# Optimization experiments

Hardware: AMD Instinct MI355X
Metric: run time of the kernel (lower is better)

## Reference

```python
import jax, jax.numpy as jnp
import numpy as np

N_HEADS = 16
KEY_DIM = 64
VAL_DIM = 64
KV_CH = 512


def setup_inputs() -> dict:
    key = jax.random.key(0)
    k1, k2, k3, k4, k5, k6 = jax.random.split(key, 6)
    B, H, W = 32, 64, 64
    kv = jax.random.normal(k1, (B, H, W, KV_CH), dtype=jnp.float32)
    # 1x1 conv kernels are just [C_in, C_out] matrices
    scale = 1.0 / np.sqrt(KV_CH)
    W_k = jax.random.normal(k2, (KV_CH, N_HEADS * KEY_DIM), dtype=jnp.float32) * scale
    b_k = jnp.zeros((N_HEADS * KEY_DIM,), dtype=jnp.float32)
    W_v = jax.random.normal(k3, (KV_CH, N_HEADS * VAL_DIM), dtype=jnp.float32) * scale
    b_v = jnp.zeros((N_HEADS * VAL_DIM,), dtype=jnp.float32)
    query = jax.random.normal(k4, (1, 1, N_HEADS, KEY_DIM), dtype=jnp.float32) * 0.05
    return {"key_value": kv, "W_k": W_k, "b_k": b_k, "W_v": W_v, "b_v": b_v, "query": query}


def reference(key_value, W_k, b_k, W_v, b_v, query):
    B, H, W, _ = key_value.shape
    HW = H * W
    x = key_value.reshape(B, HW, KV_CH)  # 1x1 conv == per-pixel matmul
    key = (jnp.einsum('bsc,cd->bsd', x, W_k) + b_k).reshape(B, HW, N_HEADS, KEY_DIM)
    value = jnp.tanh(jnp.einsum('bsc,cd->bsd', x, W_v) + b_v).reshape(B, HW, N_HEADS, VAL_DIM)
    # query broadcast dot over key dim -> [B, HW, N]
    dot = jnp.einsum('bsnk,nk->bsn', key, query[0, 0])
    attn = jax.nn.softmax(dot, axis=1)  # softmax over spatial axis
    # inference mode: dropout is identity
    out = jnp.einsum('bsn,bsnv->bnv', attn, value)  # [B, N, V]
    return out
```

## Files before the change

kernel.cpp:

```cpp
#include <hip/hip_runtime.h>
#include <cstdint>

using short8 = __attribute__((ext_vector_type(8))) short;
using f32x4  = __attribute__((ext_vector_type(4))) float;

__device__ __forceinline__ unsigned short bf16rne(float f) {
  unsigned int u = __float_as_uint(f);
  unsigned int r = u + 0x7fffu + ((u >> 16) & 1u);
  return (unsigned short)(r >> 16);
}

__device__ __forceinline__ void gl2lds16(const void* g, void* s) {
  auto gp = reinterpret_cast<const __attribute__((address_space(1))) unsigned int*>(
      reinterpret_cast<uintptr_t>(g));
  auto sp = reinterpret_cast<__attribute__((address_space(3))) unsigned int*>(
      (uint32_t)reinterpret_cast<uintptr_t>(s));
  __builtin_amdgcn_global_load_lds(gp, sp, 16, 0, 0);
}

__device__ __forceinline__ float fast_tanh(float x) {
  float e = __expf(2.0f * x);
  return 1.0f - 2.0f / (e + 1.0f);
}

__global__ void prep_kernel(const float* __restrict__ Wk, const float* __restrict__ q,
                            const float* __restrict__ Wv,
                            unsigned short* __restrict__ wqb,
                            unsigned short* __restrict__ wvt) {
  int idx = blockIdx.x * 256 + threadIdx.x;
  if (idx < 8192) {
    int n = idx >> 9, c = idx & 511;
    const float* wrow = Wk + (long)c * 1024 + n * 64;
    const float* qrow = q + n * 64;
    float s = 0.f;
    #pragma unroll 8
    for (int k = 0; k < 64; ++k) s += wrow[k] * qrow[k];
    wqb[n * 512 + c] = bf16rne(s);
  } else {
    int j = idx - 8192;
    if (j < 524288) {
      int col = j >> 9, c = j & 511;
      wvt[col * 512 + c] = bf16rne(Wv[(long)c * 1024 + col]);
    }
  }
}

__global__ void convert_kernel(const float4* __restrict__ x, ushort4* __restrict__ xb, int n4) {
  int stride = gridDim.x * blockDim.x;
  for (int i = blockIdx.x * blockDim.x + threadIdx.x; i < n4; i += stride) {
    float4 f = x[i];
    ushort4 o;
    o.x = bf16rne(f.x); o.y = bf16rne(f.y); o.z = bf16rne(f.z); o.w = bf16rne(f.w);
    xb[i] = o;
  }
}

__global__ __launch_bounds__(256) void dot_kernel(
    const unsigned short* __restrict__ xb, const unsigned short* __restrict__ wqb,
    float* __restrict__ dotbuf) {
  __shared__ __align__(16) unsigned short As[128 * 64];
  __shared__ __align__(16) unsigned short Ws[16 * 512];
  int tid = threadIdx.x;
  int l = tid & 63, w = tid >> 6;
  int lr = l >> 3, lc = l & 7;
  long row0 = (long)blockIdx.x * 128;

  for (int j = 0; j < 4; ++j) {
    int n = w * 4 + j;
    gl2lds16(wqb + n * 512 + ((l ^ (n & 7)) * 8), &Ws[n * 512]);
  }

  f32x4 acc[2];
  for (int mi = 0; mi < 2; ++mi) acc[mi] = f32x4{0.f, 0.f, 0.f, 0.f};

  for (int kb = 0; kb < 8; ++kb) {
    __syncthreads();
    for (int j = 0; j < 4; ++j) {
      int jj = w * 4 + j;
      int m = jj * 8 + lr;
      gl2lds16(xb + (row0 + m) * 512 + kb * 64 + ((lc ^ lr) * 8), &As[jj * 512]);
    }
    __syncthreads();
    #pragma unroll
    for (int k32 = 0; k32 < 2; ++k32) {
      int n = l & 15, qd = l >> 4;
      int cl = kb * 8 + k32 * 4 + qd;
      short8 bf = *(const short8*)&Ws[n * 512 + ((cl ^ (n & 7)) * 8)];
      int ch = k32 * 4 + qd;
      #pragma unroll
      for (int mi = 0; mi < 2; ++mi) {
        int m = w * 32 + mi * 16 + (l & 15);
        short8 af = *(const short8*)&As[m * 64 + ((ch ^ (l & 7)) * 8)];
        acc[mi] = __builtin_amdgcn_mfma_f32_16x16x32_bf16(af, bf, acc[mi], 0, 0, 0);
      }
    }
  }
  int n = l & 15, qd = l >> 4;
  for (int mi = 0; mi < 2; ++mi) {
    long rg = row0 + w * 32 + mi * 16 + qd * 4;
    long b = rg >> 12;
    long s = rg & 4095;
    *(f32x4*)&dotbuf[((b * 16 + n) << 12) + s] = acc[mi];
  }
}

__global__ __launch_bounds__(256) void softmax_kernel(float* __restrict__ dotbuf) {
  long bn = blockIdx.x;
  float4* p = (float4*)(dotbuf + bn * 4096);
  int tid = threadIdx.x;
  int l = tid & 63, w = tid >> 6;
  float4 v[4];
  float mx = -1e30f;
  #pragma unroll
  for (int i = 0; i < 4; ++i) {
    v[i] = p[tid + i * 256];
    mx = fmaxf(mx, fmaxf(fmaxf(v[i].x, v[i].y), fmaxf(v[i].z, v[i].w)));
  }
  for (int o = 32; o; o >>= 1) mx = fmaxf(mx, __shfl_xor(mx, o, 64));
  __shared__ float redm[4];
  __shared__ float reds[4];
  if (l == 0) redm[w] = mx;
  __syncthreads();
  mx = fmaxf(fmaxf(redm[0], redm[1]), fmaxf(redm[2], redm[3]));
  float s = 0.f;
  #pragma unroll
  for (int i = 0; i < 4; ++i) {
    v[i].x = __expf(v[i].x - mx); v[i].y = __expf(v[i].y - mx);
    v[i].z = __expf(v[i].z - mx); v[i].w = __expf(v[i].w - mx);
    s += v[i].x + v[i].y + v[i].z + v[i].w;
  }
  for (int o = 32; o; o >>= 1) s += __shfl_xor(s, o, 64);
  if (l == 0) reds[w] = s;
  __syncthreads();
  s = reds[0] + reds[1] + reds[2] + reds[3];
  float inv = 1.0f / s;
  #pragma unroll
  for (int i = 0; i < 4; ++i) {
    v[i].x *= inv; v[i].y *= inv; v[i].z *= inv; v[i].w *= inv;
    p[tid + i * 256] = v[i];
  }
}

__global__ __launch_bounds__(256) void out_gemm_kernel(
    const unsigned short* __restrict__ xb, const unsigned short* __restrict__ wvt,
    const float* __restrict__ wn, const float* __restrict__ bv,
    float* __restrict__ out) {
  __shared__ __align__(16) unsigned short As[128 * 64];
  __shared__ __align__(16) unsigned short Bs[128 * 64];
  __shared__ float wlds[256];
  int tid = threadIdx.x;
  int l = tid & 63, w = tid >> 6;
  int wr = w >> 1, wc = w & 1;
  int lr = l >> 3, lc = l & 7;
  int ct = blockIdx.x, rt = blockIdx.y, b = blockIdx.z;
  long row0 = ((long)b << 12) + rt * 128;
  long col0 = (long)ct * 128;
  const unsigned short* Ag = xb + row0 * 512;
  const unsigned short* Bg = wvt + col0 * 512;

  f32x4 acc[4][4];
  #pragma unroll
  for (int mi = 0; mi < 4; ++mi)
    #pragma unroll
    for (int ni = 0; ni < 4; ++ni) acc[mi][ni] = f32x4{0.f, 0.f, 0.f, 0.f};

  for (int kb = 0; kb < 8; ++kb) {
    __syncthreads();
    for (int j = 0; j < 4; ++j) {
      int jj = w * 4 + j;
      int r = jj * 8 + lr;
      int goff = r * 512 + kb * 64 + (lc ^ lr) * 8;
      gl2lds16(Ag + goff, &As[jj * 512]);
      gl2lds16(Bg + goff, &Bs[jj * 512]);
    }
    __syncthreads();
    #pragma unroll
    for (int k32 = 0; k32 < 2; ++k32) {
      int ch = k32 * 4 + (l >> 4);
      short8 af[4], bfr[4];
      #pragma unroll
      for (int mi = 0; mi < 4; ++mi) {
        int m = wr * 64 + mi * 16 + (l & 15);
        af[mi] = *(const short8*)&As[m * 64 + ((ch ^ (l & 7)) * 8)];
      }
      #pragma unroll
      for (int ni = 0; ni < 4; ++ni) {
        int n = wc * 64 + ni * 16 + (l & 15);
        bfr[ni] = *(const short8*)&Bs[n * 64 + ((ch ^ (l & 7)) * 8)];
      }
      #pragma unroll
      for (int mi = 0; mi < 4; ++mi)
        #pragma unroll
        for (int ni = 0; ni < 4; ++ni)
          acc[mi][ni] = __builtin_amdgcn_mfma_f32_16x16x32_bf16(af[mi], bfr[ni], acc[mi][ni], 0, 0, 0);
    }
  }

  int head0 = ct * 2;
  __syncthreads();
  {
    int hh = tid >> 7, r = tid & 127;
    wlds[tid] = wn[(((long)b * 16 + head0 + hh) << 12) + rt * 128 + r];
  }
  __syncthreads();
  int ngl = head0 + wc;
  int v0 = l & 15, qd = l >> 4;
  float bias[4];
  #pragma unroll
  for (int ni = 0; ni < 4; ++ni) bias[ni] = bv[ngl * 64 + ni * 16 + v0];
  float res[4] = {0.f, 0.f, 0.f, 0.f};
  #pragma unroll
  for (int mi = 0; mi < 4; ++mi) {
    int rb = wr * 64 + mi * 16 + qd * 4;
    float w0 = wlds[wc * 128 + rb + 0];
    float w1 = wlds[wc * 128 + rb + 1];
    float w2 = wlds[wc * 128 + rb + 2];
    float w3 = wlds[wc * 128 + rb + 3];
    #pragma unroll
    for (int ni = 0; ni < 4; ++ni) {
      f32x4 c = acc[mi][ni];
      res[ni] += w0 * fast_tanh(c[0] + bias[ni]) + w1 * fast_tanh(c[1] + bias[ni])
               + w2 * fast_tanh(c[2] + bias[ni]) + w3 * fast_tanh(c[3] + bias[ni]);
    }
  }
  #pragma unroll
  for (int ni = 0; ni < 4; ++ni) {
    float v = res[ni];
    v += __shfl_xor(v, 16, 64);
    v += __shfl_xor(v, 32, 64);
    if (qd == 0) atomicAdd(&out[b * 1024 + ngl * 64 + ni * 16 + v0], v);
  }
}

extern "C" void kernel_launch(void* const* d_in, const int* in_sizes, int n_in,
                              void* d_out, int out_size, void* d_ws, size_t ws_size,
                              hipStream_t stream) {
  const float* kv = (const float*)d_in[0];
  const float* Wk = (const float*)d_in[1];
  const float* Wv = (const float*)d_in[3];
  const float* bv = (const float*)d_in[4];
  const float* q  = (const float*)d_in[5];
  float* out = (float*)d_out;

  char* ws = (char*)d_ws;
  unsigned short* xb  = (unsigned short*)(ws);
  unsigned short* wqb = (unsigned short*)(ws + 134217728);
  unsigned short* wvt = (unsigned short*)(ws + 134217728 + 16384);
  float* dotbuf = (float*)(ws + 134217728 + 16384 + 1048576);

  hipMemsetAsync(d_out, 0, 32768 * sizeof(float), stream);
  prep_kernel<<<2081, 256, 0, stream>>>(Wk, q, Wv, wqb, wvt);
  convert_kernel<<<4096, 256, 0, stream>>>((const float4*)kv, (ushort4*)xb, 16777216);
  dot_kernel<<<1024, 256, 0, stream>>>(xb, wqb, dotbuf);
  softmax_kernel<<<512, 256, 0, stream>>>(dotbuf);
  out_gemm_kernel<<<dim3(8, 32, 32), 256, 0, stream>>>(xb, wvt, dotbuf, bv, out);
}
```

Measured before the change: 656.9 us.

## Fuse fp32-to-bf16 conversion into dot kernel, tile-transpose Wv, swizzle GEMM grid

Drops the separate convert kernel. The dot kernel now reads fp32 activations directly, converts them to bf16 in registers, writes the bf16 copy for the later GEMM, and fills LDS itself, which removes one full read of the large intermediate. The Wv transpose in prep now goes through a padded LDS tile so both its reads and writes are coalesced. The output GEMM grid is flattened and remapped so that blocks sharing the same activation rows run close together, which should improve L2 reuse. The cost is that the dot kernel loses the async global-to-LDS path and gains an extra barrier per K-step.

```diff
diff --git a/kernel.cpp b/kernel.cpp
--- a/kernel.cpp
+++ b/kernel.cpp
@@ -23,12 +23,14 @@
   return 1.0f - 2.0f / (e + 1.0f);
 }
 
-__global__ void prep_kernel(const float* __restrict__ Wk, const float* __restrict__ q,
-                            const float* __restrict__ Wv,
-                            unsigned short* __restrict__ wqb,
-                            unsigned short* __restrict__ wvt) {
-  int idx = blockIdx.x * 256 + threadIdx.x;
-  if (idx < 8192) {
+__global__ __launch_bounds__(256) void prep_kernel(
+    const float* __restrict__ Wk, const float* __restrict__ q,
+    const float* __restrict__ Wv,
+    unsigned short* __restrict__ wqb, unsigned short* __restrict__ wvt) {
+  __shared__ float T[64 * 65];
+  int bid = blockIdx.x;
+  if (bid < 32) {
+    int idx = bid * 256 + threadIdx.x;
     int n = idx >> 9, c = idx & 511;
     const float* wrow = Wk + (long)c * 1024 + n * 64;
     const float* qrow = q + n * 64;
@@ -37,32 +39,31 @@
     for (int k = 0; k < 64; ++k) s += wrow[k] * qrow[k];
     wqb[n * 512 + c] = bf16rne(s);
   } else {
-    int j = idx - 8192;
-    if (j < 524288) {
-      int col = j >> 9, c = j & 511;
-      wvt[col * 512 + c] = bf16rne(Wv[(long)c * 1024 + col]);
-    }
-  }
-}
-
-__global__ void convert_kernel(const float4* __restrict__ x, ushort4* __restrict__ xb, int n4) {
-  int stride = gridDim.x * blockDim.x;
-  for (int i = blockIdx.x * blockDim.x + threadIdx.x; i < n4; i += stride) {
-    float4 f = x[i];
-    ushort4 o;
-    o.x = bf16rne(f.x); o.y = bf16rne(f.y); o.z = bf16rne(f.z); o.w = bf16rne(f.w);
-    xb[i] = o;
+    int t = bid - 32;
+    int tc = t & 7, tl = t >> 3;
+    int c0 = tc * 64, l0 = tl * 64;
+    int j = threadIdx.x & 63, i0 = threadIdx.x >> 6;
+    #pragma unroll
+    for (int ii = 0; ii < 16; ++ii) {
+      int i = i0 * 16 + ii;
+      T[i * 65 + j] = Wv[(long)(c0 + i) * 1024 + l0 + j];
+    }
+    __syncthreads();
+    #pragma unroll
+    for (int ii = 0; ii < 16; ++ii) {
+      int jj = i0 * 16 + ii;
+      wvt[(long)(l0 + jj) * 512 + c0 + j] = bf16rne(T[j * 65 + jj]);
+    }
   }
 }
 
 __global__ __launch_bounds__(256) void dot_kernel(
-    const unsigned short* __restrict__ xb, const unsigned short* __restrict__ wqb,
-    float* __restrict__ dotbuf) {
+    const float* __restrict__ kv, const unsigned short* __restrict__ wqb,
+    unsigned short* __restrict__ xb, float* __restrict__ dotbuf) {
   __shared__ __align__(16) unsigned short As[128 * 64];
   __shared__ __align__(16) unsigned short Ws[16 * 512];
   int tid = threadIdx.x;
   int l = tid & 63, w = tid >> 6;
-  int lr = l >> 3, lc = l & 7;
   long row0 = (long)blockIdx.x * 128;
 
   for (int j = 0; j < 4; ++j) {
@@ -74,11 +75,29 @@
   for (int mi = 0; mi < 2; ++mi) acc[mi] = f32x4{0.f, 0.f, 0.f, 0.f};
 
   for (int kb = 0; kb < 8; ++kb) {
-    __syncthreads();
-    for (int j = 0; j < 4; ++j) {
-      int jj = w * 4 + j;
-      int m = jj * 8 + lr;
-      gl2lds16(xb + (row0 + m) * 512 + kb * 64 + ((lc ^ lr) * 8), &As[jj * 512]);
+    float4 fa[4][2];
+    short8 ha[4];
+    #pragma unroll
+    for (int it = 0; it < 4; ++it) {
+      int idx = it * 256 + tid;
+      int r = idx >> 3, c8 = idx & 7;
+      const float4* src = (const float4*)&kv[(row0 + r) * 512 + kb * 64 + c8 * 8];
+      fa[it][0] = src[0];
+      fa[it][1] = src[1];
+      short8 h;
+      h[0] = bf16rne(fa[it][0].x); h[1] = bf16rne(fa[it][0].y);
+      h[2] = bf16rne(fa[it][0].z); h[3] = bf16rne(fa[it][0].w);
+      h[4] = bf16rne(fa[it][1].x); h[5] = bf16rne(fa[it][1].y);
+      h[6] = bf16rne(fa[it][1].z); h[7] = bf16rne(fa[it][1].w);
+      ha[it] = h;
+      *(short8*)&xb[(row0 + r) * 512 + kb * 64 + c8 * 8] = h;
+    }
+    __syncthreads();
+    #pragma unroll
+    for (int it = 0; it < 4; ++it) {
+      int idx = it * 256 + tid;
+      int r = idx >> 3, c8 = idx & 7;
+      *(short8*)&As[r * 64 + ((c8 ^ (r & 7)) * 8)] = ha[it];
     }
     __syncthreads();
     #pragma unroll
@@ -94,6 +113,7 @@
         acc[mi] = __builtin_amdgcn_mfma_f32_16x16x32_bf16(af, bf, acc[mi], 0, 0, 0);
       }
     }
+    __syncthreads();
   }
   int n = l & 15, qd = l >> 4;
   for (int mi = 0; mi < 2; ++mi) {
@@ -152,7 +172,13 @@
   int l = tid & 63, w = tid >> 6;
   int wr = w >> 1, wc = w & 1;
   int lr = l >> 3, lc = l & 7;
-  int ct = blockIdx.x, rt = blockIdx.y, b = blockIdx.z;
+
+  int id = blockIdx.x;
+  int ct = (id >> 3) & 7;
+  int g  = (id & 7) | ((id >> 6) << 3);
+  int rt = g & 31;
+  int b  = g >> 5;
+
   long row0 = ((long)b << 12) + rt * 128;
   long col0 = (long)ct * 128;
   const unsigned short* Ag = xb + row0 * 512;
@@ -249,9 +275,8 @@
   float* dotbuf = (float*)(ws + 134217728 + 16384 + 1048576);
 
   hipMemsetAsync(d_out, 0, 32768 * sizeof(float), stream);
-  prep_kernel<<<2081, 256, 0, stream>>>(Wk, q, Wv, wqb, wvt);
-  convert_kernel<<<4096, 256, 0, stream>>>((const float4*)kv, (ushort4*)xb, 16777216);
-  dot_kernel<<<1024, 256, 0, stream>>>(xb, wqb, dotbuf);
+  prep_kernel<<<160, 256, 0, stream>>>(Wk, q, Wv, wqb, wvt);
+  dot_kernel<<<1024, 256, 0, stream>>>(kv, wqb, xb, dotbuf);
   softmax_kernel<<<512, 256, 0, stream>>>(dotbuf);
-  out_gemm_kernel<<<dim3(8, 32, 32), 256, 0, stream>>>(xb, wvt, dotbuf, bv, out);
-}
+  out_gemm_kernel<<<8192, 256, 0, stream>>>(xb, wvt, dotbuf, bv, out);
+}
```

After: 636.6 us. 3.1% less time.
